# Performance work log

Measured on AMD Instinct MI355X. Metric: run time of the kernel, lower is better.

The kernel has to match this reference:

```python
import jax, jax.numpy as jnp
import numpy as np

B, DIM, HEADS, Hs, Ws = 8, 192, 8, 128, 128


def setup_inputs() -> dict:
    key = jax.random.key(0)
    ks = jax.random.split(key, 8)
    d3 = 3 * DIM
    inp = {
        "x": jax.random.normal(ks[0], (B, DIM, Hs, Ws), dtype=jnp.float32),
        # qkv 1x1 conv: (out=3*dim, in=dim)
        "w_qkv": jax.random.normal(ks[1], (d3, DIM), dtype=jnp.float32) / np.sqrt(DIM),
        "b_qkv": jnp.zeros((d3,), dtype=jnp.float32),
        # depthwise 3x3 conv, groups = 3*dim -> kernel (3*dim, 1, 3, 3)
        "w_dw": jax.random.normal(ks[2], (d3, 1, 3, 3), dtype=jnp.float32) / 3.0,
        "b_dw": jnp.zeros((d3,), dtype=jnp.float32),
        # project_out 1x1 conv: (dim, dim)
        "w_proj": jax.random.normal(ks[3], (DIM, DIM), dtype=jnp.float32) / np.sqrt(DIM),
        "b_proj": jnp.zeros((DIM,), dtype=jnp.float32),
        "temperature": jnp.ones((HEADS, 1, 1), dtype=jnp.float32),
        "a1": jnp.full((1,), 0.2, dtype=jnp.float32),
        "a2": jnp.full((1,), 0.2, dtype=jnp.float32),
        "a3": jnp.full((1,), 0.2, dtype=jnp.float32),
        "a4": jnp.full((1,), 0.2, dtype=jnp.float32),
    }
    return inp


def _sparse_softmax(attn, k):
    # top-k per row, scatter 1s at those indices, mask rest to -inf, softmax
    _, idx = jax.lax.top_k(attn, k)                      # [..., C, k]
    C = attn.shape[-1]
    mask = jax.nn.one_hot(idx, C, dtype=attn.dtype).sum(-2)  # [..., C, C]
    masked = jnp.where(mask > 0, attn, -jnp.inf)
    return jax.nn.softmax(masked, axis=-1)


def _l2norm(t):
    # torch F.normalize: x / max(||x||_2, eps) along last axis
    n = jnp.sqrt(jnp.sum(t * t, axis=-1, keepdims=True))
    return t / jnp.maximum(n, 1e-12)


def reference(x, w_qkv, b_qkv, w_dw, b_dw, w_proj, b_proj, temperature, a1, a2, a3, a4):
    b, c, h, w = x.shape
    # 1x1 conv
    qkv = jnp.einsum('oi,bihw->bohw', w_qkv, x) + b_qkv[:, None, None]
    # depthwise 3x3 conv, padding=1
    qkv = jax.lax.conv_general_dilated(
        qkv, w_dw, window_strides=(1, 1), padding='SAME',
        feature_group_count=3 * c,
        dimension_numbers=('NCHW', 'OIHW', 'NCHW')) + b_dw[:, None, None]
    q, k, v = jnp.split(qkv, 3, axis=1)
    Cd = c // HEADS  # per-head channel dim
    heads = lambda t: t.reshape(b, HEADS, Cd, h * w)
    q, k, v = heads(q), heads(k), heads(v)
    q, k = _l2norm(q), _l2norm(k)
    # transposed (channel) attention: [b, head, Cd, Cd]
    attn = jnp.einsum('bhcn,bhdn->bhcd', q, k) * temperature
    ks = (int(Cd / 2), int(Cd * 2 / 3), int(Cd * 3 / 4), int(Cd * 4 / 5))
    out1 = jnp.einsum('bhcd,bhdn->bhcn', _sparse_softmax(attn, ks[0]), v)
    out2 = jnp.einsum('bhcd,bhdn->bhcn', _sparse_softmax(attn, ks[1]), v)
    out3 = jnp.einsum('bhcd,bhdn->bhcn', _sparse_softmax(attn, ks[2]), v)
    out4 = jnp.einsum('bhcd,bhdn->bhcn', _sparse_softmax(attn, ks[3]), v)
    out = out1 * a1 + out2 * a2 + out3 * a3 + out4 * a4
    out = out.reshape(b, c, h, w)
    out = jnp.einsum('oi,bihw->bohw', w_proj, out) + b_proj[:, None, None]
    return out
```

## Files before the change

### kernel.cpp

```cpp
#include <hip/hip_runtime.h>
#include <math.h>

#define DIMC 192
#define C3 576
#define NHEADS 8
#define CDh 24
#define HWN 16384
#define WIDTH 128
#define NBATCH 8

typedef __attribute__((ext_vector_type(8))) short short8;
typedef __attribute__((ext_vector_type(4))) float f32x4;

__device__ __forceinline__ ushort f2bf(float f) {
    uint u = __float_as_uint(f);
    u += 0x7fff + ((u >> 16) & 1);
    return (ushort)(u >> 16);
}
__device__ __forceinline__ float bf2f(ushort h) {
    return __uint_as_float(((uint)h) << 16);
}

__global__ void k0_prep(const float* __restrict__ W, ushort* __restrict__ Wh,
                        ushort* __restrict__ Wl, int n) {
    int i = blockIdx.x * 256 + threadIdx.x;
    if (i < n) {
        float w = W[i];
        ushort h = f2bf(w);
        Wh[i] = h;
        Wl[i] = f2bf(w - bf2f(h));
    }
}

__global__ __launch_bounds__(256) void k0x_tr(const float* __restrict__ x,
                                              ushort* __restrict__ xTh,
                                              ushort* __restrict__ xTl,
                                              long xT_zs, int b0) {
    __shared__ float tile[64 * 65];
    const int z = blockIdx.z;
    const float* xb = x + (size_t)(b0 + z) * DIMC * HWN;
    const int px0 = blockIdx.x * 64, ch0 = blockIdx.y * 64;
    const int tid = threadIdx.x;
#pragma unroll
    for (int it = 0; it < 16; it++) {
        int f = tid + it * 256;
        int row = f >> 6, col = f & 63;
        tile[row * 65 + col] = xb[(size_t)(ch0 + row) * HWN + px0 + col];
    }
    __syncthreads();
    uint* dh = (uint*)(xTh + (size_t)z * xT_zs);
    uint* dl = (uint*)(xTl + (size_t)z * xT_zs);
#pragma unroll
    for (int s = 0; s < 8; s++) {
        int f = tid + s * 256;
        int pxl = f >> 5, uidx = f & 31;
        float v0 = tile[(2 * uidx) * 65 + pxl];
        float v1 = tile[(2 * uidx + 1) * 65 + pxl];
        ushort h0 = f2bf(v0), h1 = f2bf(v1);
        ushort l0 = f2bf(v0 - bf2f(h0)), l1 = f2bf(v1 - bf2f(h1));
        size_t dst = (size_t)(px0 + pxl) * 96 + (ch0 >> 1) + uidx;
        dh[dst] = (uint)h0 | ((uint)h1 << 16);
        dl[dst] = (uint)l0 | ((uint)l1 << 16);
    }
}

template <int NI>
__global__ __launch_bounds__(256, 2) void kg(
    const ushort* __restrict__ Bh, const ushort* __restrict__ Bl, long B_zs,
    const ushort* __restrict__ Ah, const ushort* __restrict__ Al, long A_zs,
    const float* __restrict__ bias, float* __restrict__ out, long out_zs) {
    __shared__ ushort smem[2 * 64 * 200];
    ushort* BsH = smem;
    ushort* BsL = smem + 64 * 200;
    const int z = blockIdx.z;
    const int n0 = blockIdx.x * 64;
    const int tid = threadIdx.x;
    const ushort* sh = Bh + (size_t)z * B_zs + (size_t)n0 * DIMC;
    const ushort* sl = Bl + (size_t)z * B_zs + (size_t)n0 * DIMC;
#pragma unroll
    for (int it = 0; it < 6; it++) {
        int f = tid + it * 256;
        int px = f / 24, oct = f - px * 24;
        *(short8*)&BsH[px * 200 + oct * 8] = *(const short8*)&sh[(size_t)px * DIMC + oct * 8];
        *(short8*)&BsL[px * 200 + oct * 8] = *(const short8*)&sl[(size_t)px * DIMC + oct * 8];
    }
    __syncthreads();
    const int wid = tid >> 6, lane = tid & 63;
    const int lr = lane & 15, lk = lane >> 4;
    const int mb = wid * (NI * 16);
    const ushort* Azh = Ah + (size_t)z * A_zs;
    const ushort* Azl = Al + (size_t)z * A_zs;
    float* oz = out + (size_t)z * out_zs;
    f32x4 acc[NI][4];
#pragma unroll
    for (int i = 0; i < NI; i++)
#pragma unroll
        for (int j = 0; j < 4; j++) acc[i][j] = (f32x4)0.f;

    for (int kc6 = 0; kc6 < 6; kc6++) {
        short8 bh[4], bl[4];
#pragma unroll
        for (int j = 0; j < 4; j++) {
            int ad = (j * 16 + lr) * 200 + kc6 * 32 + lk * 8;
            bh[j] = *(const short8*)&BsH[ad];
            bl[j] = *(const short8*)&BsL[ad];
        }
#pragma unroll
        for (int i = 0; i < NI; i++) {
            size_t ao = (size_t)(mb + i * 16 + lr) * DIMC + kc6 * 32 + lk * 8;
            const short8 ah = *(const short8*)&Azh[ao];
            const short8 al = *(const short8*)&Azl[ao];
#pragma unroll
            for (int j = 0; j < 4; j++) {
                acc[i][j] = __builtin_amdgcn_mfma_f32_16x16x32_bf16(ah, bh[j], acc[i][j], 0, 0, 0);
                acc[i][j] = __builtin_amdgcn_mfma_f32_16x16x32_bf16(ah, bl[j], acc[i][j], 0, 0, 0);
                acc[i][j] = __builtin_amdgcn_mfma_f32_16x16x32_bf16(al, bh[j], acc[i][j], 0, 0, 0);
            }
        }
    }
    __syncthreads();
    float* epsb = (float*)smem + wid * (2 * 1056);
#pragma unroll
    for (int i = 0; i < NI; i++) {
        float* eps = epsb + (i & 1) * 1056;
        int rb = mb + i * 16;
#pragma unroll
        for (int j = 0; j < 4; j++)
#pragma unroll
            for (int r = 0; r < 4; r++)
                eps[(lk * 4 + r) * 66 + j * 16 + lr] = acc[i][j][r] + bias[rb + lk * 4 + r];
#pragma unroll
        for (int s = 0; s < 4; s++) {
            int rl = s * 4 + (lane >> 4);
            int c4 = (lane & 15) * 4;
            f32x4 v = *(const f32x4*)&eps[rl * 66 + c4];
            *(f32x4*)&oz[(size_t)(rb + rl) * HWN + n0 + c4] = v;
        }
    }
}

__global__ __launch_bounds__(256, 3) void kg3f(float* __restrict__ vy,
                                               const ushort* __restrict__ Mh,
                                               const ushort* __restrict__ Ml,
                                               const float* __restrict__ bias) {
    __shared__ ushort smem[2 * 64 * 200];
    ushort* BsH = smem;
    ushort* BsL = smem + 64 * 200;
    const int z = blockIdx.y;
    float* vb = vy + (size_t)z * DIMC * HWN;
    const int n0 = blockIdx.x * 64;
    const int tid = threadIdx.x;
#pragma unroll
    for (int it = 0; it < 12; it++) {
        int idx = tid + it * 256;
        int ch = idx >> 4, q = idx & 15;
        f32x4 v = *(const f32x4*)&vb[(size_t)ch * HWN + n0 + q * 4];
#pragma unroll
        for (int p = 0; p < 4; p++) {
            ushort hb = f2bf(v[p]);
            BsH[(q * 4 + p) * 200 + ch] = hb;
            BsL[(q * 4 + p) * 200 + ch] = f2bf(v[p] - bf2f(hb));
        }
    }
    __syncthreads();
    const int wid = tid >> 6, lane = tid & 63;
    const int lr = lane & 15, lk = lane >> 4;
    const int mb = wid * 48;
    const ushort* Azh = Mh + (size_t)z * DIMC * DIMC;
    const ushort* Azl = Ml + (size_t)z * DIMC * DIMC;
    f32x4 acc[3][4];
#pragma unroll
    for (int i = 0; i < 3; i++)
#pragma unroll
        for (int j = 0; j < 4; j++) acc[i][j] = (f32x4)0.f;

    for (int kc6 = 0; kc6 < 6; kc6++) {
        short8 bh[4], bl[4];
#pragma unroll
        for (int j = 0; j < 4; j++) {
            int ad = (j * 16 + lr) * 200 + kc6 * 32 + lk * 8;
            bh[j] = *(const short8*)&BsH[ad];
            bl[j] = *(const short8*)&BsL[ad];
        }
#pragma unroll
        for (int i = 0; i < 3; i++) {
            size_t ao = (size_t)(mb + i * 16 + lr) * DIMC + kc6 * 32 + lk * 8;
            const short8 ah = *(const short8*)&Azh[ao];
            const short8 al = *(const short8*)&Azl[ao];
#pragma unroll
            for (int j = 0; j < 4; j++) {
                acc[i][j] = __builtin_amdgcn_mfma_f32_16x16x32_bf16(ah, bh[j], acc[i][j], 0, 0, 0);
                acc[i][j] = __builtin_amdgcn_mfma_f32_16x16x32_bf16(ah, bl[j], acc[i][j], 0, 0, 0);
                acc[i][j] = __builtin_amdgcn_mfma_f32_16x16x32_bf16(al, bh[j], acc[i][j], 0, 0, 0);
            }
        }
    }
    __syncthreads();
    float* epsb = (float*)smem + wid * (2 * 1056);
#pragma unroll
    for (int i = 0; i < 3; i++) {
        float* eps = epsb + (i & 1) * 1056;
        int rb = mb + i * 16;
#pragma unroll
        for (int j = 0; j < 4; j++)
#pragma unroll
            for (int r = 0; r < 4; r++)
                eps[(lk * 4 + r) * 66 + j * 16 + lr] = acc[i][j][r] + bias[rb + lk * 4 + r];
#pragma unroll
        for (int s = 0; s < 4; s++) {
            int rl = s * 4 + (lane >> 4);
            int c4 = (lane & 15) * 4;
            f32x4 v = *(const f32x4*)&eps[rl * 66 + c4];
            *(f32x4*)&vb[(size_t)(rb + rl) * HWN + n0 + c4] = v;
        }
    }
}

__global__ __launch_bounds__(1024, 4) void k2_dw(const float* __restrict__ qkv0, long qkv_zs,
                                                 const float* __restrict__ wdw,
                                                 const float* __restrict__ bdw,
                                                 float* __restrict__ vout,
                                                 float* __restrict__ part, int b0) {
    __shared__ float stage[2 * 6336];
    __shared__ float qks[48 * 520];
    const int b = b0 + blockIdx.z;
    const float* qkv = qkv0 + (size_t)blockIdx.z * qkv_zs;
    const int stripe = blockIdx.x, h = blockIdx.y;
    const int tid = threadIdx.x;
    const int r0 = stripe * 4;

    const int col4 = (tid & 31) * 4;
    const int orow = (tid >> 5) & 3;
    const int cc = tid >> 7;

    auto stage_load = [&](int chunk, int buf) {
        const int g = chunk / 3, cb = (chunk % 3) * 8;
        float* sb = stage + buf * 6336;
#pragma unroll
        for (int f = tid; f < 1536; f += 1024) {
            int fc = f / 192, rem = f - fc * 192;
            int rl = rem >> 5, c4 = rem & 31;
            int gr = r0 - 1 + rl;
            int ch = g * DIMC + h * CDh + cb + fc;
            float4 v = make_float4(0.f, 0.f, 0.f, 0.f);
            if (gr >= 0 && gr < 128)
                v = *(const float4*)&qkv[(size_t)ch * HWN + gr * WIDTH + c4 * 4];
            *(float4*)&sb[(fc * 6 + rl) * 132 + c4 * 4] = v;
        }
    };

    stage_load(0, 0);
    __syncthreads();
    for (int chunk = 0; chunk < 9; chunk++) {
        const int buf = chunk & 1;
        if (chunk < 8) stage_load(chunk + 1, buf ^ 1);
        const int g = chunk / 3, cb = (chunk % 3) * 8;
        const float* sb = stage + buf * 6336;
        const int ch = g * DIMC + h * CDh + cb + cc;
        float wr[9];
#pragma unroll
        for (int t = 0; t < 9; t++) wr[t] = wdw[ch * 9 + t];
        float bsv = bdw[ch];
        float a0 = bsv, a1 = bsv, a2 = bsv, a3 = bsv;
#pragma unroll
        for (int dr = 0; dr < 3; dr++) {
            const float* row = &sb[(cc * 6 + orow + dr) * 132];
            f32x4 cen = *(const f32x4*)&row[col4];
            f32x4 lf4 = (col4 > 0) ? *(const f32x4*)&row[col4 - 4] : (f32x4)0.f;
            f32x4 rt4 = (col4 < 124) ? *(const f32x4*)&row[col4 + 4] : (f32x4)0.f;
            float left = lf4[3], right = rt4[0];
            float wA = wr[dr * 3 + 0], wB = wr[dr * 3 + 1], wC = wr[dr * 3 + 2];
            a0 = fmaf(left, wA, fmaf(cen[0], wB, fmaf(cen[1], wC, a0)));
            a1 = fmaf(cen[0], wA, fmaf(cen[1], wB, fmaf(cen[2], wC, a1)));
            a2 = fmaf(cen[1], wA, fmaf(cen[2], wB, fmaf(cen[3], wC, a2)));
            a3 = fmaf(cen[2], wA, fmaf(cen[3], wB, fmaf(right, wC, a3)));
        }
        if (g < 2) {
            float4 o4 = {a0, a1, a2, a3};
            *(float4*)&qks[(g * CDh + cb + cc) * 520 + orow * 128 + col4] = o4;
        } else {
            float4 o4 = {a0, a1, a2, a3};
            *(float4*)&vout[((size_t)b * DIMC + h * CDh + cb + cc) * HWN +
                            (size_t)(r0 + orow) * WIDTH + col4] = o4;
        }
        __syncthreads();
    }

    const int tc = tid & 3, td = (tid >> 2) & 3, tp = tid >> 4;
    float ga[6][6];
#pragma unroll
    for (int i = 0; i < 6; i++)
#pragma unroll
        for (int j = 0; j < 6; j++) ga[i][j] = 0.f;
#pragma unroll
    for (int s = 0; s < 2; s++) {
        int px = tp * 8 + s * 4;
        f32x4 qv[6], kv[6];
#pragma unroll
        for (int i = 0; i < 6; i++) qv[i] = *(const f32x4*)&qks[(tc * 6 + i) * 520 + px];
#pragma unroll
        for (int j = 0; j < 6; j++) kv[j] = *(const f32x4*)&qks[(24 + td * 6 + j) * 520 + px];
#pragma unroll
        for (int i = 0; i < 6; i++)
#pragma unroll
            for (int j = 0; j < 6; j++) {
                ga[i][j] = fmaf(qv[i][0], kv[j][0], ga[i][j]);
                ga[i][j] = fmaf(qv[i][1], kv[j][1], ga[i][j]);
                ga[i][j] = fmaf(qv[i][2], kv[j][2], ga[i][j]);
                ga[i][j] = fmaf(qv[i][3], kv[j][3], ga[i][j]);
            }
    }
#pragma unroll
    for (int i = 0; i < 6; i++)
#pragma unroll
        for (int j = 0; j < 6; j++) {
            float v = ga[i][j];
            v += __shfl_xor(v, 16, 64);
            v += __shfl_xor(v, 32, 64);
            ga[i][j] = v;
        }
    float nv = 0.f;
    int nch = 0, npg = 0;
    if (tid < 768) {
        npg = tid / 48;
        nch = tid - npg * 48;
#pragma unroll
        for (int s = 0; s < 8; s++) {
            f32x4 v = *(const f32x4*)&qks[nch * 520 + npg * 32 + s * 4];
            nv = fmaf(v[0], v[0], nv);
            nv = fmaf(v[1], v[1], nv);
            nv = fmaf(v[2], v[2], nv);
            nv = fmaf(v[3], v[3], nv);
        }
    }
    __syncthreads();
    float* gscr = qks;
    const int wave = tid >> 6;
    if ((tid & 63) < 16) {
#pragma unroll
        for (int i = 0; i < 6; i++)
#pragma unroll
            for (int j = 0; j < 6; j++)
                gscr[wave * 624 + (tc * 6 + i) * 24 + (td * 6 + j)] = ga[i][j];
    }
    if (tid < 768) gscr[npg * 624 + 576 + nch] = nv;
    __syncthreads();
    if (tid < 624) {
        float s = 0.f;
#pragma unroll
        for (int w2 = 0; w2 < 16; w2++) s += gscr[w2 * 624 + tid];
        part[((size_t)(b * NHEADS + h) * 64 + stripe) * 624 + tid] = s;
    }
}

__global__ void k34_attn(const float* __restrict__ part, const float* __restrict__ temp,
                         const float* __restrict__ a1, const float* __restrict__ a2,
                         const float* __restrict__ a3, const float* __restrict__ a4,
                         float* __restrict__ Aeff) {
    __shared__ float gbuf[624];
    int bh = blockIdx.x;
    int h = bh & 7;
    int tid = threadIdx.x;
    for (int ti = tid; ti < 624; ti += 256) {
        float s = 0.f;
        const float* p = part + (size_t)bh * 64 * 624 + ti;
#pragma unroll 4
        for (int st = 0; st < 64; st++) s += p[st * 624];
        gbuf[ti] = s;
    }
    __syncthreads();
    int r = tid;
    if (r >= CDh) return;
    float t = temp[h];
    float aw[4] = {a1[0], a2[0], a3[0], a4[0]};
    const int kks[4] = {12, 16, 18, 19};
    float qn = fmaxf(sqrtf(gbuf[576 + r]), 1e-12f);
    float av[24];
    for (int d = 0; d < 24; d++) {
        float kn = fmaxf(sqrtf(gbuf[600 + d]), 1e-12f);
        av[d] = gbuf[r * 24 + d] / (qn * kn) * t;
    }
    int rank[24];
    float m = -1e30f;
    for (int d = 0; d < 24; d++) {
        int rk = 0;
        for (int e = 0; e < 24; e++)
            rk += (av[e] > av[d]) || (av[e] == av[d] && e < d);
        rank[d] = rk;
        m = fmaxf(m, av[d]);
    }
    float ex[24], outv[24];
    for (int d = 0; d < 24; d++) { ex[d] = expf(av[d] - m); outv[d] = 0.f; }
    for (int i = 0; i < 4; i++) {
        float Z = 0.f;
        for (int d = 0; d < 24; d++) if (rank[d] < kks[i]) Z += ex[d];
        float inv = aw[i] / Z;
        for (int d = 0; d < 24; d++) if (rank[d] < kks[i]) outv[d] += ex[d] * inv;
    }
    for (int d = 0; d < 24; d++) Aeff[(bh * 24 + r) * 24 + d] = outv[d];
}

__global__ void k4b_mmat(const float* __restrict__ Wp, const float* __restrict__ Aeff,
                         ushort* __restrict__ Mh, ushort* __restrict__ Ml) {
    int b = blockIdx.x;
    int e0 = blockIdx.y * 6144;
    for (int e = e0 + threadIdx.x; e < e0 + 6144; e += 256) {
        int o = e / DIMC, j = e % DIMC;
        int h = j / CDh, d = j % CDh;
        const float* wrow = Wp + o * DIMC + h * CDh;
        const float* acol = Aeff + (size_t)((b * NHEADS + h) * CDh) * CDh + d;
        float s = 0.f;
        for (int c = 0; c < CDh; c++) s = fmaf(wrow[c], acol[c * CDh], s);
        size_t idx = ((size_t)b * DIMC + o) * DIMC + j;
        ushort hb = f2bf(s);
        Mh[idx] = hb;
        Ml[idx] = f2bf(s - bf2f(hb));
    }
}

extern "C" void kernel_launch(void* const* d_in, const int* in_sizes, int n_in,
                              void* d_out, int out_size, void* d_ws, size_t ws_size,
                              hipStream_t stream) {
    const float* x     = (const float*)d_in[0];
    const float* wqkv  = (const float*)d_in[1];
    const float* bqkv  = (const float*)d_in[2];
    const float* wdw   = (const float*)d_in[3];
    const float* bdw   = (const float*)d_in[4];
    const float* wproj = (const float*)d_in[5];
    const float* bproj = (const float*)d_in[6];
    const float* temp  = (const float*)d_in[7];
    const float* a1    = (const float*)d_in[8];
    const float* a2    = (const float*)d_in[9];
    const float* a3    = (const float*)d_in[10];
    const float* a4    = (const float*)d_in[11];
    float* out = (float*)d_out;

    float* ws = (float*)d_ws;
    const size_t fl_part = (size_t)64 * 64 * 624;
    const size_t fl_A    = (size_t)64 * 576;
    const size_t fl_M    = (size_t)NBATCH * DIMC * DIMC / 2;
    const size_t fl_W    = (size_t)C3 * DIMC / 2;
    const size_t fl_xT1  = (size_t)DIMC * HWN / 2;
    const size_t fl_qkv1 = (size_t)C3 * HWN;
    const size_t base_fl = fl_part + fl_A + 2 * fl_M + 2 * fl_W;

    auto need = [&](int nzz) -> size_t {
        return (base_fl + (size_t)nzz * (2 * fl_xT1 + fl_qkv1)) * sizeof(float);
    };
    int nz = 1;
    if (ws_size >= need(8))      nz = 8;
    else if (ws_size >= need(4)) nz = 4;
    else if (ws_size >= need(2)) nz = 2;

    size_t o = 0;
    float* part = ws + o; o += fl_part;
    float* Aeff = ws + o; o += fl_A;
    ushort* Mh  = (ushort*)(ws + o); o += fl_M;
    ushort* Ml  = (ushort*)(ws + o); o += fl_M;
    ushort* Wh  = (ushort*)(ws + o); o += fl_W;
    ushort* Wl  = (ushort*)(ws + o); o += fl_W;
    ushort* xTh = (ushort*)(ws + o); o += (size_t)nz * fl_xT1;
    ushort* xTl = (ushort*)(ws + o); o += (size_t)nz * fl_xT1;
    float* qkv  = ws + o;

    const long xT_zs  = (long)DIMC * HWN;
    const long qkv_zs = (long)fl_qkv1;

    k0_prep<<<(C3 * DIMC + 255) / 256, 256, 0, stream>>>(wqkv, Wh, Wl, C3 * DIMC);

    for (int b0 = 0; b0 < NBATCH; b0 += nz) {
        k0x_tr<<<dim3(256, 3, nz), 256, 0, stream>>>(x, xTh, xTl, xT_zs, b0);
        kg<9><<<dim3(256, 1, nz), 256, 0, stream>>>(xTh, xTl, xT_zs, Wh, Wl, 0L,
                                                    bqkv, qkv, qkv_zs);
        k2_dw<<<dim3(32, 8, nz), 1024, 0, stream>>>(qkv, qkv_zs, wdw, bdw, out, part, b0);
    }
    k34_attn<<<64, 256, 0, stream>>>(part, temp, a1, a2, a3, a4, Aeff);
    k4b_mmat<<<dim3(8, 6), 256, 0, stream>>>(wproj, Aeff, Mh, Ml);
    kg3f<<<dim3(256, 8), 256, 0, stream>>>(out, Mh, Ml, bproj);
}
```

Baseline: 514.2 us.

## Fuse x transpose and bf16 split into qkv GEMM, use nontemporal stores

Removes the separate transpose kernel that wrote hi/lo bf16 copies of x to workspace. The qkv GEMM kernel now loads fp32 x directly, splits it into hi/lo bf16 and transposes it into shared memory. This saves a full round trip of the transposed copy through global memory and one launch per batch group. It also raises the occupancy hint to 3, shrinks the workspace requirement, and uses nontemporal stores for the qkv and v outputs. The cost is scattered 2-byte LDS writes that may bank-conflict during staging, and possible register pressure with 36 accumulators at 3 blocks per SM.

```diff
diff --git a/kernel.cpp b/kernel.cpp
--- a/kernel.cpp
+++ b/kernel.cpp
@@ -32,68 +32,38 @@
     }
 }
 
-__global__ __launch_bounds__(256) void k0x_tr(const float* __restrict__ x,
-                                              ushort* __restrict__ xTh,
-                                              ushort* __restrict__ xTl,
-                                              long xT_zs, int b0) {
-    __shared__ float tile[64 * 65];
-    const int z = blockIdx.z;
-    const float* xb = x + (size_t)(b0 + z) * DIMC * HWN;
-    const int px0 = blockIdx.x * 64, ch0 = blockIdx.y * 64;
-    const int tid = threadIdx.x;
-#pragma unroll
-    for (int it = 0; it < 16; it++) {
-        int f = tid + it * 256;
-        int row = f >> 6, col = f & 63;
-        tile[row * 65 + col] = xb[(size_t)(ch0 + row) * HWN + px0 + col];
-    }
-    __syncthreads();
-    uint* dh = (uint*)(xTh + (size_t)z * xT_zs);
-    uint* dl = (uint*)(xTl + (size_t)z * xT_zs);
-#pragma unroll
-    for (int s = 0; s < 8; s++) {
-        int f = tid + s * 256;
-        int pxl = f >> 5, uidx = f & 31;
-        float v0 = tile[(2 * uidx) * 65 + pxl];
-        float v1 = tile[(2 * uidx + 1) * 65 + pxl];
-        ushort h0 = f2bf(v0), h1 = f2bf(v1);
-        ushort l0 = f2bf(v0 - bf2f(h0)), l1 = f2bf(v1 - bf2f(h1));
-        size_t dst = (size_t)(px0 + pxl) * 96 + (ch0 >> 1) + uidx;
-        dh[dst] = (uint)h0 | ((uint)h1 << 16);
-        dl[dst] = (uint)l0 | ((uint)l1 << 16);
-    }
-}
-
-template <int NI>
-__global__ __launch_bounds__(256, 2) void kg(
-    const ushort* __restrict__ Bh, const ushort* __restrict__ Bl, long B_zs,
-    const ushort* __restrict__ Ah, const ushort* __restrict__ Al, long A_zs,
-    const float* __restrict__ bias, float* __restrict__ out, long out_zs) {
+__global__ __launch_bounds__(256, 3) void kgx9(const float* __restrict__ x,
+                                               const ushort* __restrict__ Wh,
+                                               const ushort* __restrict__ Wl,
+                                               const float* __restrict__ bias,
+                                               float* __restrict__ qkv, long qkv_zs) {
     __shared__ ushort smem[2 * 64 * 200];
     ushort* BsH = smem;
     ushort* BsL = smem + 64 * 200;
     const int z = blockIdx.z;
+    const float* xb = x + (size_t)z * DIMC * HWN;
     const int n0 = blockIdx.x * 64;
     const int tid = threadIdx.x;
-    const ushort* sh = Bh + (size_t)z * B_zs + (size_t)n0 * DIMC;
-    const ushort* sl = Bl + (size_t)z * B_zs + (size_t)n0 * DIMC;
-#pragma unroll
-    for (int it = 0; it < 6; it++) {
-        int f = tid + it * 256;
-        int px = f / 24, oct = f - px * 24;
-        *(short8*)&BsH[px * 200 + oct * 8] = *(const short8*)&sh[(size_t)px * DIMC + oct * 8];
-        *(short8*)&BsL[px * 200 + oct * 8] = *(const short8*)&sl[(size_t)px * DIMC + oct * 8];
+#pragma unroll
+    for (int it = 0; it < 12; it++) {
+        int idx = tid + it * 256;
+        int ch = idx >> 4, q = idx & 15;
+        f32x4 v = *(const f32x4*)&xb[(size_t)ch * HWN + n0 + q * 4];
+#pragma unroll
+        for (int p = 0; p < 4; p++) {
+            ushort hb = f2bf(v[p]);
+            BsH[(q * 4 + p) * 200 + ch] = hb;
+            BsL[(q * 4 + p) * 200 + ch] = f2bf(v[p] - bf2f(hb));
+        }
     }
     __syncthreads();
     const int wid = tid >> 6, lane = tid & 63;
     const int lr = lane & 15, lk = lane >> 4;
-    const int mb = wid * (NI * 16);
-    const ushort* Azh = Ah + (size_t)z * A_zs;
-    const ushort* Azl = Al + (size_t)z * A_zs;
-    float* oz = out + (size_t)z * out_zs;
-    f32x4 acc[NI][4];
-#pragma unroll
-    for (int i = 0; i < NI; i++)
+    const int mb = wid * 144;
+    float* oz = qkv + (size_t)z * qkv_zs;
+    f32x4 acc[9][4];
+#pragma unroll
+    for (int i = 0; i < 9; i++)
 #pragma unroll
         for (int j = 0; j < 4; j++) acc[i][j] = (f32x4)0.f;
 
@@ -106,10 +76,10 @@
             bl[j] = *(const short8*)&BsL[ad];
         }
 #pragma unroll
-        for (int i = 0; i < NI; i++) {
+        for (int i = 0; i < 9; i++) {
             size_t ao = (size_t)(mb + i * 16 + lr) * DIMC + kc6 * 32 + lk * 8;
-            const short8 ah = *(const short8*)&Azh[ao];
-            const short8 al = *(const short8*)&Azl[ao];
+            const short8 ah = *(const short8*)&Wh[ao];
+            const short8 al = *(const short8*)&Wl[ao];
 #pragma unroll
             for (int j = 0; j < 4; j++) {
                 acc[i][j] = __builtin_amdgcn_mfma_f32_16x16x32_bf16(ah, bh[j], acc[i][j], 0, 0, 0);
@@ -121,7 +91,7 @@
     __syncthreads();
     float* epsb = (float*)smem + wid * (2 * 1056);
 #pragma unroll
-    for (int i = 0; i < NI; i++) {
+    for (int i = 0; i < 9; i++) {
         float* eps = epsb + (i & 1) * 1056;
         int rb = mb + i * 16;
 #pragma unroll
@@ -134,7 +104,7 @@
             int rl = s * 4 + (lane >> 4);
             int c4 = (lane & 15) * 4;
             f32x4 v = *(const f32x4*)&eps[rl * 66 + c4];
-            *(f32x4*)&oz[(size_t)(rb + rl) * HWN + n0 + c4] = v;
+            __builtin_nontemporal_store(v, (f32x4*)&oz[(size_t)(rb + rl) * HWN + n0 + c4]);
         }
     }
 }
@@ -279,9 +249,10 @@
             float4 o4 = {a0, a1, a2, a3};
             *(float4*)&qks[(g * CDh + cb + cc) * 520 + orow * 128 + col4] = o4;
         } else {
-            float4 o4 = {a0, a1, a2, a3};
-            *(float4*)&vout[((size_t)b * DIMC + h * CDh + cb + cc) * HWN +
-                            (size_t)(r0 + orow) * WIDTH + col4] = o4;
+            f32x4 o4 = {a0, a1, a2, a3};
+            __builtin_nontemporal_store(
+                o4, (f32x4*)&vout[((size_t)b * DIMC + h * CDh + cb + cc) * HWN +
+                                  (size_t)(r0 + orow) * WIDTH + col4]);
         }
         __syncthreads();
     }
@@ -440,12 +411,11 @@
     const size_t fl_A    = (size_t)64 * 576;
     const size_t fl_M    = (size_t)NBATCH * DIMC * DIMC / 2;
     const size_t fl_W    = (size_t)C3 * DIMC / 2;
-    const size_t fl_xT1  = (size_t)DIMC * HWN / 2;
     const size_t fl_qkv1 = (size_t)C3 * HWN;
     const size_t base_fl = fl_part + fl_A + 2 * fl_M + 2 * fl_W;
 
     auto need = [&](int nzz) -> size_t {
-        return (base_fl + (size_t)nzz * (2 * fl_xT1 + fl_qkv1)) * sizeof(float);
+        return (base_fl + (size_t)nzz * fl_qkv1) * sizeof(float);
     };
     int nz = 1;
     if (ws_size >= need(8))      nz = 8;
@@ -459,19 +429,15 @@
     ushort* Ml  = (ushort*)(ws + o); o += fl_M;
     ushort* Wh  = (ushort*)(ws + o); o += fl_W;
     ushort* Wl  = (ushort*)(ws + o); o += fl_W;
-    ushort* xTh = (ushort*)(ws + o); o += (size_t)nz * fl_xT1;
-    ushort* xTl = (ushort*)(ws + o); o += (size_t)nz * fl_xT1;
     float* qkv  = ws + o;
 
-    const long xT_zs  = (long)DIMC * HWN;
     const long qkv_zs = (long)fl_qkv1;
 
     k0_prep<<<(C3 * DIMC + 255) / 256, 256, 0, stream>>>(wqkv, Wh, Wl, C3 * DIMC);
 
     for (int b0 = 0; b0 < NBATCH; b0 += nz) {
-        k0x_tr<<<dim3(256, 3, nz), 256, 0, stream>>>(x, xTh, xTl, xT_zs, b0);
-        kg<9><<<dim3(256, 1, nz), 256, 0, stream>>>(xTh, xTl, xT_zs, Wh, Wl, 0L,
-                                                    bqkv, qkv, qkv_zs);
+        kgx9<<<dim3(256, 1, nz), 256, 0, stream>>>(x + (size_t)b0 * DIMC * HWN,
+                                                   Wh, Wl, bqkv, qkv, qkv_zs);
         k2_dw<<<dim3(32, 8, nz), 1024, 0, stream>>>(qkv, qkv_zs, wdw, bdw, out, part, b0);
     }
     k34_attn<<<64, 256, 0, stream>>>(part, temp, a1, a2, a3, a4, Aeff);
```

New measurement: 649.6 us. 26.3% more time.
